# Kernel optimization log

Measured on AMD Instinct MI355X. Metric: run time of the kernel, lower is better.

## Reference

```python
import jax, jax.numpy as jnp
import numpy as np

# dims
H = 1024          # hidden_size
E = 2048          # d_inner = 2*H
NH = 32           # nheads = E/64
P = 64            # headdim
N = 128           # d_state
G = 1             # ngroups
K = 4             # d_conv
Q = 128           # SSD chunk length
FF = 4096         # intermediate_size
EPS = 1e-6        # rms_norm_eps
NEPS = 1e-5       # mamba gated-norm eps
CONV_DIM = E + 2 * G * N            # 2304
D_IN = 2 * E + 2 * G * N + NH       # 4384


def rmsnorm(x, w, eps):
    v = jnp.mean(x.astype(jnp.float32) ** 2, axis=-1, keepdims=True)
    return (x.astype(jnp.float32) * jax.lax.rsqrt(v + eps)).astype(x.dtype) * w


def segsum(x):
    # x: [..., T] -> [..., T, T] with out[i,j] = sum_{j<k<=i} x[k], -inf above diag
    T = x.shape[-1]
    cs = jnp.cumsum(x, axis=-1)
    s = cs[..., :, None] - cs[..., None, :]
    mask = jnp.tril(jnp.ones((T, T), dtype=bool))
    return jnp.where(mask, s, -jnp.inf)


def ssd(x, dt, A_log, B, C):
    # x:[b,l,nh,p], dt:[b,l,nh], B,C:[b,l,N] (ngroups=1, shared over heads)
    b, l, nh, p = x.shape
    A = -jnp.exp(A_log)                      # [nh]
    dA = dt * A                              # [b,l,nh]
    xd = x * dt[..., None]                   # discretized input
    c = l // Q
    xd = xd.reshape(b, c, Q, nh, p)
    dAc = dA.reshape(b, c, Q, nh).transpose(0, 3, 1, 2)   # [b,h,c,q]
    Bc = B.reshape(b, c, Q, N)
    Cc = C.reshape(b, c, Q, N)
    A_cs = jnp.cumsum(dAc, axis=-1)                        # [b,h,c,q]
    Lm = jnp.exp(segsum(dAc))                              # [b,h,c,q,q]
    # intra-chunk (diagonal blocks)
    Y_diag = jnp.einsum('bcqn,bcsn,bhcqs,bcshp->bcqhp', Cc, Bc, Lm, xd)
    # per-chunk final states
    decay_states = jnp.exp(A_cs[..., -1:] - A_cs)          # [b,h,c,q]
    states = jnp.einsum('bcqn,bhcq,bcqhp->bchpn', Bc, decay_states, xd)
    # inter-chunk recurrence (initial state = 0)
    A_last = jnp.pad(A_cs[..., -1], ((0, 0), (0, 0), (1, 0)))   # [b,h,c+1]
    decay_chunk = jnp.exp(segsum(A_last))                       # [b,h,c+1,c+1]
    states = jnp.concatenate([jnp.zeros_like(states[:, :1]), states], axis=1)
    new_states = jnp.einsum('bhzc,bchpn->bzhpn', decay_chunk, states)[:, :-1]
    Y_off = jnp.einsum('bcqn,bchpn,bhcq->bcqhp', Cc, new_states, jnp.exp(A_cs))
    return (Y_diag + Y_off).reshape(b, l, nh, p)


def mamba2(h, w_in, w_conv, b_conv, dt_bias, A_log, D, w_mnorm, w_out):
    b, l, _ = h.shape
    zxbcdt = h @ w_in.T                         # [b,l,D_IN]
    z, xBC, dt = jnp.split(zxbcdt, [E, E + CONV_DIM], axis=-1)
    # causal depthwise conv (kernel K) over channels of xBC
    pad = jnp.pad(xBC, ((0, 0), (K - 1, 0), (0, 0)))
    xBC = sum(pad[:, k:k + l, :] * w_conv[:, k] for k in range(K)) + b_conv
    xBC = jax.nn.silu(xBC)
    x, B, C = jnp.split(xBC, [E, E + G * N], axis=-1)
    dt = jax.nn.softplus(dt + dt_bias)          # [b,l,NH]
    xh = x.reshape(b, l, NH, P)
    y = ssd(xh, dt, A_log, B, C)
    y = y + D[None, None, :, None] * xh         # per-head skip
    y = y.reshape(b, l, E)
    y = rmsnorm(y * jax.nn.silu(z), w_mnorm, NEPS)   # gated RMSNorm
    return y @ w_out.T


def setup_inputs() -> dict:
    key = jax.random.key(0)
    ks = jax.random.split(key, 12)
    dt0 = jax.random.uniform(ks[0], (NH,), minval=0.001, maxval=0.1)
    dt_bias = dt0 + jnp.log(-jnp.expm1(-dt0))   # inverse softplus
    return {
        'hidden_states': jax.random.normal(ks[1], (2, 2048, H), dtype=jnp.float32),
        'w_ln1': jnp.ones((H,), jnp.float32),
        'w_in': 0.02 * jax.random.normal(ks[2], (D_IN, H), dtype=jnp.float32),
        'w_conv': 0.1 * jax.random.normal(ks[3], (CONV_DIM, K), dtype=jnp.float32),
        'b_conv': jnp.zeros((CONV_DIM,), jnp.float32),
        'dt_bias': dt_bias,
        'A_log': jnp.log(jax.random.uniform(ks[4], (NH,), minval=1.0, maxval=16.0)),
        'D': jnp.ones((NH,), jnp.float32),
        'w_mnorm': jnp.ones((E,), jnp.float32),
        'w_out': 0.02 * jax.random.normal(ks[5], (H, E), dtype=jnp.float32),
        'w_ln2': jnp.ones((H,), jnp.float32),
        'w_gate': 0.02 * jax.random.normal(ks[6], (FF, H), dtype=jnp.float32),
        'w_up': 0.02 * jax.random.normal(ks[7], (FF, H), dtype=jnp.float32),
        'w_down': 0.02 * jax.random.normal(ks[8], (H, FF), dtype=jnp.float32),
    }


def reference(hidden_states, w_ln1, w_in, w_conv, b_conv, dt_bias, A_log, D,
              w_mnorm, w_out, w_ln2, w_gate, w_up, w_down):
    residual = hidden_states
    h = rmsnorm(hidden_states, w_ln1, EPS)
    h = mamba2(h, w_in, w_conv, b_conv, dt_bias, A_log, D, w_mnorm, w_out)
    hidden = residual + h
    residual = hidden
    h = rmsnorm(hidden, w_ln2, EPS)
    h = (jax.nn.silu(h @ w_gate.T) * (h @ w_up.T)) @ w_down.T
    return residual + h
```

## Files before the change

### kernel.cpp

```cpp
#include <hip/hip_runtime.h>

#define DEV static __device__ __forceinline__

typedef short bf16x8 __attribute__((ext_vector_type(8)));
typedef float floatx4 __attribute__((ext_vector_type(4)));
typedef unsigned short ushort4v __attribute__((ext_vector_type(4)));
typedef unsigned short ushort8v __attribute__((ext_vector_type(8)));

DEV unsigned short f32_bf16(float f) {
  unsigned int u = __builtin_bit_cast(unsigned int, f);
  u = u + 0x7fffu + ((u >> 16) & 1u);
  return (unsigned short)(u >> 16);
}
DEV float bf2f(unsigned short u) {
  unsigned int v = ((unsigned int)u) << 16;
  return __builtin_bit_cast(float, v);
}
DEV float sigmoidf_(float x) { return 1.0f / (1.0f + __expf(-x)); }
DEV float siluf_(float x) { return x * sigmoidf_(x); }

#define GLD_LDS16(g, l)                                                              \
  __builtin_amdgcn_global_load_lds((const __attribute__((address_space(1))) void*)(g), \
                                   (__attribute__((address_space(3))) void*)(l), 16, 0, 0)

template <int MODE>
__global__ __launch_bounds__(256) void gemm128(
    const unsigned short* __restrict__ A, const unsigned short* __restrict__ B,
    void* __restrict__ Cv, const unsigned short* __restrict__ other,
    int K, int lda, int ldb, int ldc, long long bsA, long long bsB, long long bsC) {
  __shared__ unsigned short As[128 * 32];
  __shared__ unsigned short Bs[128 * 32];
  A += (long long)blockIdx.z * bsA;
  B += (long long)blockIdx.z * bsB;
  const long long coff = (long long)blockIdx.z * bsC;
  const int tid = threadIdx.x;
  const int w = tid >> 6, lane = tid & 63;

  const int nbx = gridDim.x, nby = gridDim.y;
  const int GM = 4;
  int bid = blockIdx.y * nbx + blockIdx.x;
  int gid = bid / (GM * nbx);
  int rem = bid - gid * (GM * nbx);
  int gsz = min(GM, nby - gid * GM);
  int mtile = gid * GM + rem % gsz;
  int ntile = rem / gsz;
  const int m0 = mtile << 7, n0 = ntile << 7;

  const int srow = lane >> 2;
  const int schunk = ((lane & 3) ^ (srow & 3)) * 8;
  const unsigned short* ag0 = A + (long long)(m0 + w * 32 + srow) * lda + schunk;
  const unsigned short* ag1 = ag0 + (long long)16 * lda;
  const unsigned short* bg0 = B + (long long)(n0 + w * 32 + srow) * ldb + schunk;
  const unsigned short* bg1 = bg0 + (long long)16 * ldb;
  unsigned short* al0 = As + (w * 32) * 32 + lane * 8;
  unsigned short* al1 = As + (w * 32 + 16) * 32 + lane * 8;
  unsigned short* bl0 = Bs + (w * 32) * 32 + lane * 8;
  unsigned short* bl1 = Bs + (w * 32 + 16) * 32 + lane * 8;

  const int wr = (w >> 1) << 6, wc = (w & 1) << 6;
  const int fr = lane & 15;
  const int slot = (((lane >> 4) ^ (fr & 3))) << 3;

  floatx4 acc[4][4];
#pragma unroll
  for (int i = 0; i < 4; ++i)
#pragma unroll
    for (int j = 0; j < 4; ++j) acc[i][j] = (floatx4){0.f, 0.f, 0.f, 0.f};

  for (int k0 = 0; k0 < K; k0 += 32) {
    __syncthreads();
    GLD_LDS16(ag0 + k0, al0);
    GLD_LDS16(ag1 + k0, al1);
    GLD_LDS16(bg0 + k0, bl0);
    GLD_LDS16(bg1 + k0, bl1);
    __syncthreads();
    bf16x8 af[4], bf_[4];
#pragma unroll
    for (int i = 0; i < 4; ++i)
      af[i] = *(const bf16x8*)(As + (wr + i * 16 + fr) * 32 + slot);
#pragma unroll
    for (int j = 0; j < 4; ++j)
      bf_[j] = *(const bf16x8*)(Bs + (wc + j * 16 + fr) * 32 + slot);
#pragma unroll
    for (int i = 0; i < 4; ++i)
#pragma unroll
      for (int j = 0; j < 4; ++j)
        acc[i][j] = __builtin_amdgcn_mfma_f32_16x16x32_bf16(af[i], bf_[j], acc[i][j], 0, 0, 0);
  }

  const int r0 = (lane >> 4) << 2;
#pragma unroll
  for (int i = 0; i < 4; ++i) {
#pragma unroll
    for (int j = 0; j < 4; ++j) {
      long long base = (long long)(m0 + wr + i * 16 + r0) * ldc + (n0 + wc + j * 16 + fr);
#pragma unroll
      for (int r = 0; r < 4; ++r) {
        long long idx = coff + base + (long long)r * ldc;
        float v = acc[i][j][r];
        if constexpr (MODE == 0) {
          ((float*)Cv)[idx] = v;
        } else if constexpr (MODE == 1) {
          ((unsigned short*)Cv)[idx] = f32_bf16(v);
        } else {
          ((unsigned short*)Cv)[idx] = f32_bf16(siluf_(v) * bf2f(other[idx]));
        }
      }
    }
  }
}

template <int WM>
__global__ __launch_bounds__(256) void gemm_small_nt(
    const unsigned short* __restrict__ A, const unsigned short* __restrict__ B,
    float* __restrict__ C, int M, int N, int K, int lda, int ldb, int ldc) {
  const int w = threadIdx.x >> 6;
  const int lane = threadIdx.x & 63;
  const int lm = lane & 15;
  const int ko = (lane >> 4) << 3;
  const int bn0 = blockIdx.x << 6;
  const int m_base = blockIdx.y * (WM * 64) + w * (WM * 16);

  const unsigned short* arow[WM];
#pragma unroll
  for (int i = 0; i < WM; ++i) arow[i] = A + (long long)(m_base + i * 16 + lm) * lda + ko;
  int nv = (N - bn0) >> 4;
  nv = nv > 4 ? 4 : nv;
  const unsigned short* brow[4];
#pragma unroll
  for (int j = 0; j < 4; ++j) {
    int nr = bn0 + j * 16 + lm;
    brow[j] = B + (long long)(j < nv ? nr : 0) * ldb + ko;
  }
  floatx4 acc[WM][4];
#pragma unroll
  for (int i = 0; i < WM; ++i)
#pragma unroll
    for (int j = 0; j < 4; ++j) acc[i][j] = (floatx4){0.f, 0.f, 0.f, 0.f};
  for (int k0 = 0; k0 < K; k0 += 32) {
    bf16x8 a[WM];
#pragma unroll
    for (int i = 0; i < WM; ++i) a[i] = *(const bf16x8*)(arow[i] + k0);
#pragma unroll
    for (int j = 0; j < 4; ++j) {
      if (j < nv) {
        bf16x8 b = *(const bf16x8*)(brow[j] + k0);
#pragma unroll
        for (int i = 0; i < WM; ++i)
          acc[i][j] = __builtin_amdgcn_mfma_f32_16x16x32_bf16(a[i], b, acc[i][j], 0, 0, 0);
      }
    }
  }
  const int r0 = (lane >> 4) << 2;
#pragma unroll
  for (int i = 0; i < WM; ++i)
#pragma unroll
    for (int j = 0; j < 4; ++j)
      if (j < nv) {
        int col = bn0 + j * 16 + lm;
        long long base = (long long)(m_base + i * 16 + r0) * ldc + col;
#pragma unroll
        for (int r = 0; r < 4; ++r) C[base + (long long)r * ldc] = acc[i][j][r];
      }
}

__global__ __launch_bounds__(256) void f32_to_bf16_k(const float* __restrict__ src,
                                                     unsigned short* __restrict__ dst,
                                                     long long n4) {
  long long i = (long long)blockIdx.x * 256 + threadIdx.x;
  if (i < n4) {
    float4 v = ((const float4*)src)[i];
    ushort4v o = {f32_bf16(v.x), f32_bf16(v.y), f32_bf16(v.z), f32_bf16(v.w)};
    ((ushort4v*)dst)[i] = o;
  }
}

__global__ __launch_bounds__(256) void zero_out_k(float* __restrict__ o, long long n) {
  long long i = (long long)blockIdx.x * 256 + threadIdx.x;
  if (i < n) o[i] = 0.f;
}

__global__ __launch_bounds__(256) void rmsnorm1024_bf16_k(const float* __restrict__ x,
                                                          const float* __restrict__ w,
                                                          unsigned short* __restrict__ out,
                                                          float eps) {
  long long row = blockIdx.x;
  int t = threadIdx.x;
  float4 v = ((const float4*)(x + row * 1024))[t];
  float ss = v.x * v.x + v.y * v.y + v.z * v.z + v.w * v.w;
  __shared__ float red[4];
#pragma unroll
  for (int o = 32; o > 0; o >>= 1) ss += __shfl_down(ss, o, 64);
  if ((t & 63) == 0) red[t >> 6] = ss;
  __syncthreads();
  float tot = red[0] + red[1] + red[2] + red[3];
  float sc = rsqrtf(tot * (1.0f / 1024.0f) + eps);
  float4 wv = ((const float4*)w)[t];
  ushort4v o = {f32_bf16(v.x * sc * wv.x), f32_bf16(v.y * sc * wv.y),
                f32_bf16(v.z * sc * wv.z), f32_bf16(v.w * sc * wv.w)};
  ((ushort4v*)(out + row * 1024))[t] = o;
}

__global__ __launch_bounds__(256) void add_rmsnorm_k(const float* __restrict__ hs,
                                                     const float* __restrict__ parts,
                                                     long long pstride, int np,
                                                     const float* __restrict__ w,
                                                     float* __restrict__ mh,
                                                     unsigned short* __restrict__ h2, float eps) {
  long long row = blockIdx.x;
  int t = threadIdx.x;
  float4 v = ((const float4*)(hs + row * 1024))[t];
  for (int p = 0; p < np; ++p) {
    float4 u = ((const float4*)(parts + p * pstride + row * 1024))[t];
    v.x += u.x;
    v.y += u.y;
    v.z += u.z;
    v.w += u.w;
  }
  ((float4*)(mh + row * 1024))[t] = v;
  float ss = v.x * v.x + v.y * v.y + v.z * v.z + v.w * v.w;
  __shared__ float red[4];
#pragma unroll
  for (int o = 32; o > 0; o >>= 1) ss += __shfl_down(ss, o, 64);
  if ((t & 63) == 0) red[t >> 6] = ss;
  __syncthreads();
  float tot = red[0] + red[1] + red[2] + red[3];
  float sc = rsqrtf(tot * (1.0f / 1024.0f) + eps);
  float4 wv = ((const float4*)w)[t];
  ushort4v o = {f32_bf16(v.x * sc * wv.x), f32_bf16(v.y * sc * wv.y),
                f32_bf16(v.z * sc * wv.z), f32_bf16(v.w * sc * wv.w)};
  ((ushort4v*)(h2 + row * 1024))[t] = o;
}

__global__ __launch_bounds__(256) void addn_f32_k(const float* __restrict__ a,
                                                  const float* __restrict__ parts,
                                                  long long pstride, int np,
                                                  float* __restrict__ o, long long n4) {
  long long i = (long long)blockIdx.x * 256 + threadIdx.x;
  if (i < n4) {
    float4 x = ((const float4*)a)[i];
    for (int p = 0; p < np; ++p) {
      float4 u = ((const float4*)(parts + p * pstride))[i];
      x.x += u.x;
      x.y += u.y;
      x.z += u.z;
      x.w += u.w;
    }
    ((float4*)o)[i] = x;
  }
}

__global__ __launch_bounds__(256) void gated_rmsnorm2048_k(const unsigned short* __restrict__ y,
                                                           const unsigned short* __restrict__ z,
                                                           const float* __restrict__ w,
                                                           unsigned short* __restrict__ out,
                                                           float eps) {
  long long row = blockIdx.x;
  int t = threadIdx.x;
  ushort8v yv = ((const ushort8v*)(y + row * 2048))[t];
  ushort8v zv = ((const ushort8v*)(z + row * 2048))[t];
  float g[8];
  float ss = 0.f;
#pragma unroll
  for (int j = 0; j < 8; ++j) {
    g[j] = bf2f(yv[j]) * siluf_(bf2f(zv[j]));
    ss += g[j] * g[j];
  }
  __shared__ float red[4];
#pragma unroll
  for (int o = 32; o > 0; o >>= 1) ss += __shfl_down(ss, o, 64);
  if ((t & 63) == 0) red[t >> 6] = ss;
  __syncthreads();
  float tot = red[0] + red[1] + red[2] + red[3];
  float sc = rsqrtf(tot * (1.0f / 2048.0f) + eps);
  float ww[8];
  *(float4*)&ww[0] = ((const float4*)w)[2 * t];
  *(float4*)&ww[4] = ((const float4*)w)[2 * t + 1];
  ushort8v o;
#pragma unroll
  for (int j = 0; j < 8; ++j) o[j] = f32_bf16(g[j] * sc * ww[j]);
  ((ushort8v*)(out + row * 2048))[t] = o;
}

__global__ __launch_bounds__(256) void conv_silu_k(const unsigned short* __restrict__ xraw,
                                                   const float* __restrict__ wconv,
                                                   const float* __restrict__ bconv,
                                                   unsigned short* __restrict__ xBC) {
  int m = blockIdx.x;
  int l = m & 2047;
  for (int ch = threadIdx.x; ch < 2304; ch += 256) {
    float acc = bconv[ch];
#pragma unroll
    for (int k = 0; k < 4; ++k) {
      int lk = l + k - 3;
      if (lk >= 0) acc += bf2f(xraw[(long long)(m + k - 3) * 2304 + ch]) * wconv[ch * 4 + k];
    }
    xBC[(long long)m * 2304 + ch] = f32_bf16(siluf_(acc));
  }
}

__global__ __launch_bounds__(256) void dt_softplus_k(const float* __restrict__ dtraw,
                                                     const float* __restrict__ dt_bias,
                                                     float* __restrict__ dt_s) {
  int i = blockIdx.x * 256 + threadIdx.x;
  float xv = dtraw[i] + dt_bias[i & 31];
  dt_s[i] = xv > 20.f ? xv : log1pf(expf(xv));
}

__global__ __launch_bounds__(128) void dA_cumsum_k(const float* __restrict__ dt_s,
                                                   const float* __restrict__ A_log,
                                                   float* __restrict__ dA_cs) {
  int bi = blockIdx.x;
  int c = bi & 15, h = (bi >> 4) & 31, b = bi >> 9;
  int q = threadIdx.x;
  float A = -expf(A_log[h]);
  float v = dt_s[((long long)(b * 2048 + c * 128 + q)) * 32 + h] * A;
  __shared__ float sbuf[128];
  sbuf[q] = v;
  __syncthreads();
  for (int off = 1; off < 128; off <<= 1) {
    float tv = (q >= off) ? sbuf[q - off] : 0.f;
    __syncthreads();
    sbuf[q] += tv;
    __syncthreads();
  }
  dA_cs[(long long)bi * 128 + q] = sbuf[q];
}

__global__ __launch_bounds__(256) void ssd_diag_states_k(
    const unsigned short* __restrict__ xBC, const float* __restrict__ dt_s,
    const float* __restrict__ dA_cs, const unsigned short* __restrict__ G,
    unsigned short* __restrict__ y, unsigned short* __restrict__ states) {
  __shared__ unsigned short Mz[128 * 136];
  __shared__ unsigned short xdT[64 * 136];
  __shared__ float Acs[128];
  __shared__ float wdec[128];
  const int bx = blockIdx.x;
  const int h = bx & 31, c = (bx >> 5) & 15, b = bx >> 9;
  const int t = threadIdx.x;
  const int w = t >> 6, lane = t & 63, fr = lane & 15, hi = lane >> 4;
  const long long rowbase = (long long)b * 2048 + c * 128;
  const long long abase = ((long long)((b * 32 + h) * 16 + c)) << 7;

  if (t < 128) {
    float a = dA_cs[abase + t];
    Acs[t] = a;
    wdec[t] = __expf(dA_cs[abase + 127] - a);
  }
  {
    int s = t >> 1, p0 = (t & 1) * 32;
    float dtv = dt_s[(rowbase + s) * 32 + h];
    const ushort8v* xv = (const ushort8v*)(xBC + (rowbase + s) * 2304 + h * 64 + p0);
#pragma unroll
    for (int i = 0; i < 4; ++i) {
      ushort8v vv = xv[i];
#pragma unroll
      for (int j = 0; j < 8; ++j) xdT[(p0 + i * 8 + j) * 136 + s] = f32_bf16(bf2f(vv[j]) * dtv);
    }
  }
  __syncthreads();
  {
    int q = t >> 1, s0 = (t & 1) * 64;
    float aq = Acs[q];
    const ushort8v* gv =
        (const ushort8v*)(G + (((long long)(b * 16 + c)) * 128 + q) * 128 + s0);
#pragma unroll
    for (int i = 0; i < 8; ++i) {
      ushort8v gg = gv[i];
#pragma unroll
      for (int j = 0; j < 8; ++j) {
        int s = s0 + i * 8 + j;
        float m = (s <= q) ? bf2f(gg[j]) * __expf(aq - Acs[s]) : 0.f;
        Mz[q * 136 + s] = f32_bf16(m);
      }
    }
  }
  __syncthreads();
  const int q0 = w << 5;
  {
    floatx4 acc[2][4];
#pragma unroll
    for (int i = 0; i < 2; ++i)
#pragma unroll
      for (int j = 0; j < 4; ++j) acc[i][j] = (floatx4){0.f, 0.f, 0.f, 0.f};
#pragma unroll
    for (int k0 = 0; k0 < 128; k0 += 32) {
      int kk = k0 + hi * 8;
      bf16x8 a0 = *(const bf16x8*)(Mz + (q0 + fr) * 136 + kk);
      bf16x8 a1 = *(const bf16x8*)(Mz + (q0 + 16 + fr) * 136 + kk);
      bf16x8 bf_[4];
#pragma unroll
      for (int j = 0; j < 4; ++j) bf_[j] = *(const bf16x8*)(xdT + (j * 16 + fr) * 136 + kk);
#pragma unroll
      for (int j = 0; j < 4; ++j) {
        acc[0][j] = __builtin_amdgcn_mfma_f32_16x16x32_bf16(a0, bf_[j], acc[0][j], 0, 0, 0);
        acc[1][j] = __builtin_amdgcn_mfma_f32_16x16x32_bf16(a1, bf_[j], acc[1][j], 0, 0, 0);
      }
    }
#pragma unroll
    for (int i = 0; i < 2; ++i)
#pragma unroll
      for (int r = 0; r < 4; ++r) {
        int q = q0 + i * 16 + hi * 4 + r;
        unsigned short* yrow = y + (rowbase + q) * 2048 + h * 64;
#pragma unroll
        for (int j = 0; j < 4; ++j) yrow[j * 16 + fr] = f32_bf16(acc[i][j][r]);
      }
  }
  __syncthreads();
  {
    int s = t >> 1, n0 = (t & 1) * 64;
    float wd = wdec[s];
    const ushort8v* bv = (const ushort8v*)(xBC + (rowbase + s) * 2304 + 2048 + n0);
#pragma unroll
    for (int i = 0; i < 8; ++i) {
      ushort8v bb = bv[i];
#pragma unroll
      for (int j = 0; j < 8; ++j) Mz[(n0 + i * 8 + j) * 136 + s] = f32_bf16(bf2f(bb[j]) * wd);
    }
  }
  __syncthreads();
  {
    floatx4 acc[2][4];
#pragma unroll
    for (int i = 0; i < 2; ++i)
#pragma unroll
      for (int j = 0; j < 4; ++j) acc[i][j] = (floatx4){0.f, 0.f, 0.f, 0.f};
#pragma unroll
    for (int k0 = 0; k0 < 128; k0 += 32) {
      int kk = k0 + hi * 8;
      bf16x8 a0 = *(const bf16x8*)(Mz + (q0 + fr) * 136 + kk);
      bf16x8 a1 = *(const bf16x8*)(Mz + (q0 + 16 + fr) * 136 + kk);
      bf16x8 bf_[4];
#pragma unroll
      for (int j = 0; j < 4; ++j) bf_[j] = *(const bf16x8*)(xdT + (j * 16 + fr) * 136 + kk);
#pragma unroll
      for (int j = 0; j < 4; ++j) {
        acc[0][j] = __builtin_amdgcn_mfma_f32_16x16x32_bf16(a0, bf_[j], acc[0][j], 0, 0, 0);
        acc[1][j] = __builtin_amdgcn_mfma_f32_16x16x32_bf16(a1, bf_[j], acc[1][j], 0, 0, 0);
      }
    }
    unsigned short* st = states + (long long)bx * 8192;
#pragma unroll
    for (int i = 0; i < 2; ++i)
#pragma unroll
      for (int j = 0; j < 4; ++j) {
        int p = j * 16 + fr;
        int n = q0 + i * 16 + hi * 4;
        ushort4v o;
#pragma unroll
        for (int r = 0; r < 4; ++r) o[r] = f32_bf16(acc[i][j][r]);
        *(ushort4v*)(st + p * 128 + n) = o;
      }
  }
}

__global__ __launch_bounds__(256) void ssd_scan_k(const float* __restrict__ dA_cs,
                                                  unsigned short* __restrict__ states) {
  int h = blockIdx.x & 31, b = blockIdx.x >> 5;
  int t = threadIdx.x;
  float carry[32];
#pragma unroll
  for (int i = 0; i < 32; ++i) carry[i] = 0.f;
  for (int c = 0; c < 16; ++c) {
    long long base = ((long long)((b * 16 + c) * 32 + h)) * 8192;
    float dec = __expf(dA_cs[(((long long)((b * 32 + h) * 16 + c)) << 7) + 127]);
#pragma unroll
    for (int i = 0; i < 32; ++i) {
      long long idx = base + t + i * 256;
      float local = bf2f(states[idx]);
      states[idx] = f32_bf16(carry[i]);
      carry[i] = dec * carry[i] + local;
    }
  }
}

__global__ __launch_bounds__(256) void ssd_off_k(const unsigned short* __restrict__ xBC,
                                                 const float* __restrict__ dA_cs,
                                                 const unsigned short* __restrict__ states,
                                                 const float* __restrict__ Dvec,
                                                 unsigned short* __restrict__ y) {
  __shared__ float eA[128];
  const int bx = blockIdx.x;
  const int h = bx & 31, c = (bx >> 5) & 15, b = bx >> 9;
  const int t = threadIdx.x;
  const int w = t >> 6, lane = t & 63, fr = lane & 15, hi = lane >> 4;
  const long long rowbase = (long long)b * 2048 + c * 128;
  const long long abase = ((long long)((b * 32 + h) * 16 + c)) << 7;
  if (t < 128) eA[t] = __expf(dA_cs[abase + t]);
  __syncthreads();

  const unsigned short* st = states + (long long)bx * 8192;
  const int q0 = w << 5;
  floatx4 acc[2][4];
#pragma unroll
  for (int i = 0; i < 2; ++i)
#pragma unroll
    for (int j = 0; j < 4; ++j) acc[i][j] = (floatx4){0.f, 0.f, 0.f, 0.f};

#pragma unroll
  for (int k0 = 0; k0 < 128; k0 += 32) {
    int kk = k0 + hi * 8;
    bf16x8 a0 = *(const bf16x8*)(xBC + (rowbase + q0 + fr) * 2304 + 2176 + kk);
    bf16x8 a1 = *(const bf16x8*)(xBC + (rowbase + q0 + 16 + fr) * 2304 + 2176 + kk);
    bf16x8 bf_[4];
#pragma unroll
    for (int j = 0; j < 4; ++j) bf_[j] = *(const bf16x8*)(st + (j * 16 + fr) * 128 + kk);
#pragma unroll
    for (int j = 0; j < 4; ++j) {
      acc[0][j] = __builtin_amdgcn_mfma_f32_16x16x32_bf16(a0, bf_[j], acc[0][j], 0, 0, 0);
      acc[1][j] = __builtin_amdgcn_mfma_f32_16x16x32_bf16(a1, bf_[j], acc[1][j], 0, 0, 0);
    }
  }

  float Dh = Dvec[h];
#pragma unroll
  for (int i = 0; i < 2; ++i) {
#pragma unroll
    for (int r = 0; r < 4; ++r) {
      int q = q0 + i * 16 + hi * 4 + r;
      float e = eA[q];
      const unsigned short* xrow = xBC + (rowbase + q) * 2304 + h * 64;
      unsigned short* yrow = y + (rowbase + q) * 2048 + h * 64;
#pragma unroll
      for (int j = 0; j < 4; ++j) {
        int p = j * 16 + fr;
        float v = bf2f(yrow[p]) + e * acc[i][j][r] + Dh * bf2f(xrow[p]);
        yrow[p] = f32_bf16(v);
      }
    }
  }
}

extern "C" void kernel_launch(void* const* d_in, const int* in_sizes, int n_in, void* d_out,
                              int out_size, void* d_ws, size_t ws_size, hipStream_t stream) {
  const float* hs = (const float*)d_in[0];
  const float* w_ln1 = (const float*)d_in[1];
  const float* w_in = (const float*)d_in[2];
  const float* w_conv = (const float*)d_in[3];
  const float* b_conv = (const float*)d_in[4];
  const float* dt_bias = (const float*)d_in[5];
  const float* A_log = (const float*)d_in[6];
  const float* Dvec = (const float*)d_in[7];
  const float* w_mnorm = (const float*)d_in[8];
  const float* w_out = (const float*)d_in[9];
  const float* w_ln2 = (const float*)d_in[10];
  const float* w_gate = (const float*)d_in[11];
  const float* w_up = (const float*)d_in[12];
  const float* w_down = (const float*)d_in[13];
  float* out = (float*)d_out;
  const int M = 4096;

  char* ws = (char*)d_ws;
  const size_t R0 = 0;
  const size_t R1 = 33554432;
  const size_t R1b = R1 + 33554432;
  const size_t R2 = 71303168;
  const size_t R3 = 90177536;
  const size_t R4 = 107544576;
  const size_t W0 = 108068864;
  const size_t NEED = 133234688;

  if (ws_size < NEED) {
    hipLaunchKernelGGL(zero_out_k, dim3((out_size + 255) / 256), dim3(256), 0, stream, out,
                       (long long)out_size);
    return;
  }

  unsigned short* z = (unsigned short*)(ws + R0);
  unsigned short* act = (unsigned short*)(ws + R0);
  float* oproj_parts = (float*)(ws + R0);
  unsigned short* xraw = (unsigned short*)(ws + R1);
  unsigned short* states = (unsigned short*)(ws + R1);
  unsigned short* ybuf = (unsigned short*)(ws + R1 + 16777216);
  unsigned short* upo = (unsigned short*)(ws + R1);
  float* down_parts = (float*)(ws + R1);
  unsigned short* wbf_out = (unsigned short*)(ws + R1b);
  unsigned short* xBC = (unsigned short*)(ws + R2);
  unsigned short* ygn = (unsigned short*)(ws + R2);
  unsigned short* h2 = (unsigned short*)(ws + R2);
  unsigned short* hnorm = (unsigned short*)(ws + R3);
  unsigned short* wbf_in = (unsigned short*)(ws + R3 + 8388608);
  float* dt_s = (float*)(ws + R3);
  float* dA_cs = (float*)(ws + R3 + 524288);
  unsigned short* Gbuf = (unsigned short*)(ws + R3 + 1048576);
  float* mh = (float*)(ws + R3);
  float* dtraw = (float*)(ws + R4);
  unsigned short* wbf_gate = (unsigned short*)(ws + W0);
  unsigned short* wbf_up = (unsigned short*)(ws + W0 + 8388608);
  unsigned short* wbf_down = (unsigned short*)(ws + W0 + 16777216);

  hipLaunchKernelGGL(rmsnorm1024_bf16_k, dim3(M), dim3(256), 0, stream, hs, w_ln1, hnorm, 1e-6f);
  hipLaunchKernelGGL(f32_to_bf16_k, dim3(4384), dim3(256), 0, stream, w_in, wbf_in, 1122304LL);
  hipLaunchKernelGGL(f32_to_bf16_k, dim3(4096), dim3(256), 0, stream, w_gate, wbf_gate, 1048576LL);
  hipLaunchKernelGGL(f32_to_bf16_k, dim3(4096), dim3(256), 0, stream, w_up, wbf_up, 1048576LL);
  hipLaunchKernelGGL(f32_to_bf16_k, dim3(4096), dim3(256), 0, stream, w_down, wbf_down, 1048576LL);
  hipLaunchKernelGGL((gemm128<1>), dim3(16, 32, 1), dim3(256), 0, stream, hnorm, wbf_in, (void*)z,
                     (const unsigned short*)nullptr, 1024, 1024, 1024, 2048, 0LL, 0LL, 0LL);
  hipLaunchKernelGGL((gemm128<1>), dim3(18, 32, 1), dim3(256), 0, stream, hnorm,
                     wbf_in + 2048 * 1024, (void*)xraw, (const unsigned short*)nullptr, 1024, 1024,
                     1024, 2304, 0LL, 0LL, 0LL);
  hipLaunchKernelGGL((gemm_small_nt<4>), dim3(1, 16, 1), dim3(256), 0, stream, hnorm,
                     wbf_in + 4352 * 1024, dtraw, M, 32, 1024, 1024, 1024, 32);
  hipLaunchKernelGGL(conv_silu_k, dim3(M), dim3(256), 0, stream, xraw, w_conv, b_conv, xBC);
  hipLaunchKernelGGL(f32_to_bf16_k, dim3(2048), dim3(256), 0, stream, w_out, wbf_out, 524288LL);
  hipLaunchKernelGGL(dt_softplus_k, dim3(512), dim3(256), 0, stream, dtraw, dt_bias, dt_s);
  hipLaunchKernelGGL(dA_cumsum_k, dim3(1024), dim3(128), 0, stream, dt_s, A_log, dA_cs);
  hipLaunchKernelGGL((gemm128<1>), dim3(1, 1, 32), dim3(256), 0, stream, xBC + 2176, xBC + 2048,
                     (void*)Gbuf, (const unsigned short*)nullptr, 128, 2304, 2304, 128, 294912LL,
                     294912LL, 16384LL);
  hipLaunchKernelGGL(ssd_diag_states_k, dim3(1024), dim3(256), 0, stream, xBC, dt_s, dA_cs, Gbuf,
                     ybuf, states);
  hipLaunchKernelGGL(ssd_scan_k, dim3(64), dim3(256), 0, stream, dA_cs, states);
  hipLaunchKernelGGL(ssd_off_k, dim3(1024), dim3(256), 0, stream, xBC, dA_cs, states, Dvec, ybuf);
  hipLaunchKernelGGL(gated_rmsnorm2048_k, dim3(M), dim3(256), 0, stream, ybuf, z, w_mnorm, ygn,
                     1e-5f);
  hipLaunchKernelGGL((gemm128<0>), dim3(8, 32, 4), dim3(256), 0, stream, ygn, wbf_out,
                     (void*)oproj_parts, (const unsigned short*)nullptr, 512, 2048, 2048, 1024,
                     512LL, 512LL, 4194304LL);
  hipLaunchKernelGGL(add_rmsnorm_k, dim3(M), dim3(256), 0, stream, hs, oproj_parts, 4194304LL, 4,
                     w_ln2, mh, h2, 1e-6f);
  hipLaunchKernelGGL((gemm128<1>), dim3(32, 32, 1), dim3(256), 0, stream, h2, wbf_up, (void*)upo,
                     (const unsigned short*)nullptr, 1024, 1024, 1024, 4096, 0LL, 0LL, 0LL);
  hipLaunchKernelGGL((gemm128<2>), dim3(32, 32, 1), dim3(256), 0, stream, h2, wbf_gate, (void*)act,
                     upo, 1024, 1024, 1024, 4096, 0LL, 0LL, 0LL);
  hipLaunchKernelGGL((gemm128<0>), dim3(8, 32, 2), dim3(256), 0, stream, act, wbf_down,
                     (void*)down_parts, (const unsigned short*)nullptr, 2048, 4096, 4096, 1024,
                     2048LL, 2048LL, 4194304LL);
  hipLaunchKernelGGL(addn_f32_k, dim3(4096), dim3(256), 0, stream, mh, down_parts, 4194304LL, 2,
                     out, 1048576LL);
}
```

Baseline: 613.9 us.

## Fuse gate/up GEMMs into one GLU kernel, merge in-proj GEMMs, use K=64 stages

Gate and up projections now run in one kernel that shares the A tile and computes silu(gate)*up in the epilogue, so the bf16 up-projection intermediate is never written to memory and read back. The z and xBC in-projection GEMMs are merged into a single launch that routes output columns to two buffers. All GEMMs now stage K=64 per barrier pair instead of 32, halving synchronizations at the cost of doubling LDS use. The GLU kernel carries two accumulator sets, which raises register pressure and may lower occupancy.

```diff
diff --git a/kernel.cpp b/kernel.cpp
--- a/kernel.cpp
+++ b/kernel.cpp
@@ -26,10 +26,11 @@
 template <int MODE>
 __global__ __launch_bounds__(256) void gemm128(
     const unsigned short* __restrict__ A, const unsigned short* __restrict__ B,
-    void* __restrict__ Cv, const unsigned short* __restrict__ other,
-    int K, int lda, int ldb, int ldc, long long bsA, long long bsB, long long bsC) {
-  __shared__ unsigned short As[128 * 32];
-  __shared__ unsigned short Bs[128 * 32];
+    void* __restrict__ Cv, int K, int lda, int ldb, int ldc,
+    long long bsA, long long bsB, long long bsC,
+    int nsplit, unsigned short* __restrict__ Cv2, int ldc2) {
+  __shared__ unsigned short As[8192];
+  __shared__ unsigned short Bs[8192];
   A += (long long)blockIdx.z * bsA;
   B += (long long)blockIdx.z * bsB;
   const long long coff = (long long)blockIdx.z * bsC;
@@ -67,25 +68,143 @@
 #pragma unroll
     for (int j = 0; j < 4; ++j) acc[i][j] = (floatx4){0.f, 0.f, 0.f, 0.f};
 
-  for (int k0 = 0; k0 < K; k0 += 32) {
+  for (int k0 = 0; k0 < K; k0 += 64) {
     __syncthreads();
     GLD_LDS16(ag0 + k0, al0);
     GLD_LDS16(ag1 + k0, al1);
+    GLD_LDS16(ag0 + k0 + 32, al0 + 4096);
+    GLD_LDS16(ag1 + k0 + 32, al1 + 4096);
     GLD_LDS16(bg0 + k0, bl0);
     GLD_LDS16(bg1 + k0, bl1);
+    GLD_LDS16(bg0 + k0 + 32, bl0 + 4096);
+    GLD_LDS16(bg1 + k0 + 32, bl1 + 4096);
     __syncthreads();
-    bf16x8 af[4], bf_[4];
-#pragma unroll
-    for (int i = 0; i < 4; ++i)
-      af[i] = *(const bf16x8*)(As + (wr + i * 16 + fr) * 32 + slot);
-#pragma unroll
-    for (int j = 0; j < 4; ++j)
-      bf_[j] = *(const bf16x8*)(Bs + (wc + j * 16 + fr) * 32 + slot);
-#pragma unroll
-    for (int i = 0; i < 4; ++i)
-#pragma unroll
-      for (int j = 0; j < 4; ++j)
-        acc[i][j] = __builtin_amdgcn_mfma_f32_16x16x32_bf16(af[i], bf_[j], acc[i][j], 0, 0, 0);
+#pragma unroll
+    for (int s = 0; s < 2; ++s) {
+      const unsigned short* Ab = As + s * 4096;
+      const unsigned short* Bb = Bs + s * 4096;
+      bf16x8 af[4], bf_[4];
+#pragma unroll
+      for (int i = 0; i < 4; ++i) af[i] = *(const bf16x8*)(Ab + (wr + i * 16 + fr) * 32 + slot);
+#pragma unroll
+      for (int j = 0; j < 4; ++j) bf_[j] = *(const bf16x8*)(Bb + (wc + j * 16 + fr) * 32 + slot);
+#pragma unroll
+      for (int i = 0; i < 4; ++i)
+#pragma unroll
+        for (int j = 0; j < 4; ++j)
+          acc[i][j] = __builtin_amdgcn_mfma_f32_16x16x32_bf16(af[i], bf_[j], acc[i][j], 0, 0, 0);
+    }
+  }
+
+  const int r0 = (lane >> 4) << 2;
+#pragma unroll
+  for (int i = 0; i < 4; ++i) {
+#pragma unroll
+    for (int j = 0; j < 4; ++j) {
+      int col = n0 + wc + j * 16 + fr;
+      int row = m0 + wr + i * 16 + r0;
+#pragma unroll
+      for (int r = 0; r < 4; ++r) {
+        float v = acc[i][j][r];
+        if constexpr (MODE == 0) {
+          ((float*)Cv)[coff + (long long)(row + r) * ldc + col] = v;
+        } else {
+          if (col < nsplit)
+            ((unsigned short*)Cv)[coff + (long long)(row + r) * ldc + col] = f32_bf16(v);
+          else
+            Cv2[(long long)(row + r) * ldc2 + (col - nsplit)] = f32_bf16(v);
+        }
+      }
+    }
+  }
+}
+
+__global__ __launch_bounds__(256) void gemm128_glu(
+    const unsigned short* __restrict__ A, const unsigned short* __restrict__ Bg,
+    const unsigned short* __restrict__ Bu, unsigned short* __restrict__ act,
+    int K, int lda, int ldb, int ldc) {
+  __shared__ unsigned short As[8192];
+  __shared__ unsigned short Bgs[8192];
+  __shared__ unsigned short Bus[8192];
+  const int tid = threadIdx.x;
+  const int w = tid >> 6, lane = tid & 63;
+
+  const int nbx = gridDim.x, nby = gridDim.y;
+  const int GM = 4;
+  int bid = blockIdx.y * nbx + blockIdx.x;
+  int gid = bid / (GM * nbx);
+  int rem = bid - gid * (GM * nbx);
+  int gsz = min(GM, nby - gid * GM);
+  int mtile = gid * GM + rem % gsz;
+  int ntile = rem / gsz;
+  const int m0 = mtile << 7, n0 = ntile << 7;
+
+  const int srow = lane >> 2;
+  const int schunk = ((lane & 3) ^ (srow & 3)) * 8;
+  const unsigned short* ag0 = A + (long long)(m0 + w * 32 + srow) * lda + schunk;
+  const unsigned short* ag1 = ag0 + (long long)16 * lda;
+  const unsigned short* gg0 = Bg + (long long)(n0 + w * 32 + srow) * ldb + schunk;
+  const unsigned short* gg1 = gg0 + (long long)16 * ldb;
+  const unsigned short* ug0 = Bu + (long long)(n0 + w * 32 + srow) * ldb + schunk;
+  const unsigned short* ug1 = ug0 + (long long)16 * ldb;
+  unsigned short* al0 = As + (w * 32) * 32 + lane * 8;
+  unsigned short* al1 = As + (w * 32 + 16) * 32 + lane * 8;
+  unsigned short* gl0 = Bgs + (w * 32) * 32 + lane * 8;
+  unsigned short* gl1 = Bgs + (w * 32 + 16) * 32 + lane * 8;
+  unsigned short* ul0 = Bus + (w * 32) * 32 + lane * 8;
+  unsigned short* ul1 = Bus + (w * 32 + 16) * 32 + lane * 8;
+
+  const int wr = (w >> 1) << 6, wc = (w & 1) << 6;
+  const int fr = lane & 15;
+  const int slot = (((lane >> 4) ^ (fr & 3))) << 3;
+
+  floatx4 accg[4][4], accu[4][4];
+#pragma unroll
+  for (int i = 0; i < 4; ++i)
+#pragma unroll
+    for (int j = 0; j < 4; ++j) {
+      accg[i][j] = (floatx4){0.f, 0.f, 0.f, 0.f};
+      accu[i][j] = (floatx4){0.f, 0.f, 0.f, 0.f};
+    }
+
+  for (int k0 = 0; k0 < K; k0 += 64) {
+    __syncthreads();
+    GLD_LDS16(ag0 + k0, al0);
+    GLD_LDS16(ag1 + k0, al1);
+    GLD_LDS16(ag0 + k0 + 32, al0 + 4096);
+    GLD_LDS16(ag1 + k0 + 32, al1 + 4096);
+    GLD_LDS16(gg0 + k0, gl0);
+    GLD_LDS16(gg1 + k0, gl1);
+    GLD_LDS16(gg0 + k0 + 32, gl0 + 4096);
+    GLD_LDS16(gg1 + k0 + 32, gl1 + 4096);
+    GLD_LDS16(ug0 + k0, ul0);
+    GLD_LDS16(ug1 + k0, ul1);
+    GLD_LDS16(ug0 + k0 + 32, ul0 + 4096);
+    GLD_LDS16(ug1 + k0 + 32, ul1 + 4096);
+    __syncthreads();
+#pragma unroll
+    for (int s = 0; s < 2; ++s) {
+      const unsigned short* Ab = As + s * 4096;
+      const unsigned short* Gb = Bgs + s * 4096;
+      const unsigned short* Ub = Bus + s * 4096;
+      bf16x8 af[4], bf_[4];
+#pragma unroll
+      for (int i = 0; i < 4; ++i) af[i] = *(const bf16x8*)(Ab + (wr + i * 16 + fr) * 32 + slot);
+#pragma unroll
+      for (int j = 0; j < 4; ++j) bf_[j] = *(const bf16x8*)(Gb + (wc + j * 16 + fr) * 32 + slot);
+#pragma unroll
+      for (int i = 0; i < 4; ++i)
+#pragma unroll
+        for (int j = 0; j < 4; ++j)
+          accg[i][j] = __builtin_amdgcn_mfma_f32_16x16x32_bf16(af[i], bf_[j], accg[i][j], 0, 0, 0);
+#pragma unroll
+      for (int j = 0; j < 4; ++j) bf_[j] = *(const bf16x8*)(Ub + (wc + j * 16 + fr) * 32 + slot);
+#pragma unroll
+      for (int i = 0; i < 4; ++i)
+#pragma unroll
+        for (int j = 0; j < 4; ++j)
+          accu[i][j] = __builtin_amdgcn_mfma_f32_16x16x32_bf16(af[i], bf_[j], accu[i][j], 0, 0, 0);
+    }
   }
 
   const int r0 = (lane >> 4) << 2;
@@ -95,17 +214,8 @@
     for (int j = 0; j < 4; ++j) {
       long long base = (long long)(m0 + wr + i * 16 + r0) * ldc + (n0 + wc + j * 16 + fr);
 #pragma unroll
-      for (int r = 0; r < 4; ++r) {
-        long long idx = coff + base + (long long)r * ldc;
-        float v = acc[i][j][r];
-        if constexpr (MODE == 0) {
-          ((float*)Cv)[idx] = v;
-        } else if constexpr (MODE == 1) {
-          ((unsigned short*)Cv)[idx] = f32_bf16(v);
-        } else {
-          ((unsigned short*)Cv)[idx] = f32_bf16(siluf_(v) * bf2f(other[idx]));
-        }
-      }
+      for (int r = 0; r < 4; ++r)
+        act[base + (long long)r * ldc] = f32_bf16(siluf_(accg[i][j][r]) * accu[i][j][r]);
     }
   }
 }
@@ -550,6 +660,7 @@
   const float* w_down = (const float*)d_in[13];
   float* out = (float*)d_out;
   const int M = 4096;
+  const int NOSPLIT = 1 << 30;
 
   char* ws = (char*)d_ws;
   const size_t R0 = 0;
@@ -573,7 +684,6 @@
   unsigned short* xraw = (unsigned short*)(ws + R1);
   unsigned short* states = (unsigned short*)(ws + R1);
   unsigned short* ybuf = (unsigned short*)(ws + R1 + 16777216);
-  unsigned short* upo = (unsigned short*)(ws + R1);
   float* down_parts = (float*)(ws + R1);
   unsigned short* wbf_out = (unsigned short*)(ws + R1b);
   unsigned short* xBC = (unsigned short*)(ws + R2);
@@ -595,11 +705,8 @@
   hipLaunchKernelGGL(f32_to_bf16_k, dim3(4096), dim3(256), 0, stream, w_gate, wbf_gate, 1048576LL);
   hipLaunchKernelGGL(f32_to_bf16_k, dim3(4096), dim3(256), 0, stream, w_up, wbf_up, 1048576LL);
   hipLaunchKernelGGL(f32_to_bf16_k, dim3(4096), dim3(256), 0, stream, w_down, wbf_down, 1048576LL);
-  hipLaunchKernelGGL((gemm128<1>), dim3(16, 32, 1), dim3(256), 0, stream, hnorm, wbf_in, (void*)z,
-                     (const unsigned short*)nullptr, 1024, 1024, 1024, 2048, 0LL, 0LL, 0LL);
-  hipLaunchKernelGGL((gemm128<1>), dim3(18, 32, 1), dim3(256), 0, stream, hnorm,
-                     wbf_in + 2048 * 1024, (void*)xraw, (const unsigned short*)nullptr, 1024, 1024,
-                     1024, 2304, 0LL, 0LL, 0LL);
+  hipLaunchKernelGGL((gemm128<1>), dim3(34, 32, 1), dim3(256), 0, stream, hnorm, wbf_in, (void*)z,
+                     1024, 1024, 1024, 2048, 0LL, 0LL, 0LL, 2048, xraw, 2304);
   hipLaunchKernelGGL((gemm_small_nt<4>), dim3(1, 16, 1), dim3(256), 0, stream, hnorm,
                      wbf_in + 4352 * 1024, dtraw, M, 32, 1024, 1024, 1024, 32);
   hipLaunchKernelGGL(conv_silu_k, dim3(M), dim3(256), 0, stream, xraw, w_conv, b_conv, xBC);
@@ -607,8 +714,8 @@
   hipLaunchKernelGGL(dt_softplus_k, dim3(512), dim3(256), 0, stream, dtraw, dt_bias, dt_s);
   hipLaunchKernelGGL(dA_cumsum_k, dim3(1024), dim3(128), 0, stream, dt_s, A_log, dA_cs);
   hipLaunchKernelGGL((gemm128<1>), dim3(1, 1, 32), dim3(256), 0, stream, xBC + 2176, xBC + 2048,
-                     (void*)Gbuf, (const unsigned short*)nullptr, 128, 2304, 2304, 128, 294912LL,
-                     294912LL, 16384LL);
+                     (void*)Gbuf, 128, 2304, 2304, 128, 294912LL, 294912LL, 16384LL, NOSPLIT,
+                     (unsigned short*)nullptr, 0);
   hipLaunchKernelGGL(ssd_diag_states_k, dim3(1024), dim3(256), 0, stream, xBC, dt_s, dA_cs, Gbuf,
                      ybuf, states);
   hipLaunchKernelGGL(ssd_scan_k, dim3(64), dim3(256), 0, stream, dA_cs, states);
@@ -616,17 +723,15 @@
   hipLaunchKernelGGL(gated_rmsnorm2048_k, dim3(M), dim3(256), 0, stream, ybuf, z, w_mnorm, ygn,
                      1e-5f);
   hipLaunchKernelGGL((gemm128<0>), dim3(8, 32, 4), dim3(256), 0, stream, ygn, wbf_out,
-                     (void*)oproj_parts, (const unsigned short*)nullptr, 512, 2048, 2048, 1024,
-                     512LL, 512LL, 4194304LL);
+                     (void*)oproj_parts, 512, 2048, 2048, 1024, 512LL, 512LL, 4194304LL, NOSPLIT,
+                     (unsigned short*)nullptr, 0);
   hipLaunchKernelGGL(add_rmsnorm_k, dim3(M), dim3(256), 0, stream, hs, oproj_parts, 4194304LL, 4,
                      w_ln2, mh, h2, 1e-6f);
-  hipLaunchKernelGGL((gemm128<1>), dim3(32, 32, 1), dim3(256), 0, stream, h2, wbf_up, (void*)upo,
-                     (const unsigned short*)nullptr, 1024, 1024, 1024, 4096, 0LL, 0LL, 0LL);
-  hipLaunchKernelGGL((gemm128<2>), dim3(32, 32, 1), dim3(256), 0, stream, h2, wbf_gate, (void*)act,
-                     upo, 1024, 1024, 1024, 4096, 0LL, 0LL, 0LL);
+  hipLaunchKernelGGL(gemm128_glu, dim3(32, 32, 1), dim3(256), 0, stream, h2, wbf_gate, wbf_up, act,
+                     1024, 1024, 1024, 4096);
   hipLaunchKernelGGL((gemm128<0>), dim3(8, 32, 2), dim3(256), 0, stream, act, wbf_down,
-                     (void*)down_parts, (const unsigned short*)nullptr, 2048, 4096, 4096, 1024,
-                     2048LL, 2048LL, 4194304LL);
+                     (void*)down_parts, 2048, 4096, 4096, 1024, 2048LL, 2048LL, 4194304LL, NOSPLIT,
+                     (unsigned short*)nullptr, 0);
   hipLaunchKernelGGL(addn_f32_k, dim3(4096), dim3(256), 0, stream, mh, down_parts, 4194304LL, 2,
                      out, 1048576LL);
 }
```

Measured after the change: 625.5 us. No clear change (+1.9%).
